# Kernel optimization log

Measured on AMD Instinct MI355X. Metric: run time of the kernel, lower is better.

Reference implementation:

```python
import jax, jax.numpy as jnp
import numpy as np

NU, NI, NR = 50000, 50000, 5   # users, items, rating levels
D, B, LS, LI = 64, 512, 32, 64 # embed_dim, batch, max social nbrs, max item hist
NEG = -1e9


def setup_inputs() -> dict:
    key = jax.random.key(0)
    ks = iter(jax.random.split(key, 64))
    def lin(din, dout):
        s = 1.0 / np.sqrt(din)
        return (jax.random.uniform(next(ks), (din, dout), minval=-s, maxval=s, dtype=jnp.float32),
                jax.random.uniform(next(ks), (dout,), minval=-s, maxval=s, dtype=jnp.float32))
    inp = {}
    inp['user_w'] = jax.random.normal(next(ks), (NU, D), dtype=jnp.float32) * 0.1
    inp['item_w'] = jax.random.normal(next(ks), (NI, D), dtype=jnp.float32) * 0.1
    inp['rating_w'] = jax.random.normal(next(ks), (NR, D), dtype=jnp.float32) * 0.1
    for name, din, dout in [('i_ln1', 2*D, D), ('i_ln2', D, D), ('i_ln3', 2*D, D),
                            ('i_att1', 2*D, D), ('i_att2', D, D), ('i_att3', D, 1),
                            ('s_ln1', D, D), ('s_ln2', 2*D, D), ('s_ln3', D, D),
                            ('s_att1', 2*D, D), ('s_att2', D, D), ('s_att3', D, 1)]:
        w, b = lin(din, dout)
        inp[name + '_w'] = w
        inp[name + '_b'] = b
    inp['nodes'] = jax.random.randint(next(ks), (B,), 0, NU)
    inp['social_hist'] = jax.random.randint(next(ks), (NU, LS), 0, NU)
    inp['social_mask'] = jax.random.bernoulli(next(ks), 0.5, (NU, LS)).at[:, 0].set(True)
    inp['item_hist'] = jax.random.randint(next(ks), (NU, LI), 0, NI)
    inp['rating_hist'] = jax.random.randint(next(ks), (NU, LI), 0, NR)
    inp['item_mask'] = jax.random.bernoulli(next(ks), 0.5, (NU, LI)).at[:, 0].set(True)
    return inp


def reference(user_w, item_w, rating_w,
              i_ln1_w, i_ln1_b, i_ln2_w, i_ln2_b, i_ln3_w, i_ln3_b,
              i_att1_w, i_att1_b, i_att2_w, i_att2_b, i_att3_w, i_att3_b,
              s_ln1_w, s_ln1_b, s_ln2_w, s_ln2_b, s_ln3_w, s_ln3_b,
              s_att1_w, s_att1_b, s_att2_w, s_att2_b, s_att3_w, s_att3_b,
              nodes, social_hist, social_mask, item_hist, rating_hist, item_mask):
    relu = jax.nn.relu

    def attn(x, w1, b1, w2, b2, w3, b3, mask):
        # x: [..., L, 2D] -> softmax weights over valid neighbors: [..., L]
        h = relu(x @ w1 + b1)
        h = relu(h @ w2 + b2)
        logit = (h @ w3 + b3)[..., 0]
        logit = jnp.where(mask, logit, NEG)
        return jax.nn.softmax(logit, axis=-1)

    def item_final(uids):
        # uids: any shape [...]; returns [..., D]  (Aggre_item.item_final)
        its, rts, m = item_hist[uids], rating_hist[uids], item_mask[uids]
        x = jnp.concatenate([item_w[its], rating_w[rts]], axis=-1)   # [...,LI,2D]
        x = relu(x @ i_ln1_w + i_ln1_b)                              # [...,LI,D]
        u = user_w[uids]                                             # [...,D]
        a_in = jnp.concatenate([x, jnp.broadcast_to(u[..., None, :], x.shape)], axis=-1)
        alpha = attn(a_in, i_att1_w, i_att1_b, i_att2_w, i_att2_b, i_att3_w, i_att3_b, m)
        hI = jnp.einsum('...l,...ld->...d', alpha, x)                # attention-weighted sum
        hI = relu(hI @ i_ln2_w + i_ln2_b)
        return relu(jnp.concatenate([u, hI], axis=-1) @ i_ln3_w + i_ln3_b)

    # item-space factor of query users
    hI_self = item_final(nodes)                                      # [B,D]
    # social aggregation: item_final over each user's social neighbors
    nbrs, nmask = social_hist[nodes], social_mask[nodes]             # [B,LS]
    hI_nb = item_final(nbrs)                                         # [B,LS,D]
    u = user_w[nodes]                                                # [B,D]
    b_in = jnp.concatenate([hI_nb, jnp.broadcast_to(u[:, None, :], hI_nb.shape)], axis=-1)
    beta = attn(b_in, s_att1_w, s_att1_b, s_att2_w, s_att2_b, s_att3_w, s_att3_b, nmask)
    hS = jnp.einsum('bl,bld->bd', beta, hI_nb)
    hS = relu(hS @ s_ln1_w + s_ln1_b)
    f = jnp.concatenate([hI_self, hS], axis=-1)
    f = relu(f @ s_ln2_w + s_ln2_b)
    return relu(f @ s_ln3_w + s_ln3_b)
```

## Files before the change

kernel.cpp:

```cpp
#include <hip/hip_runtime.h>
#include <math.h>


#define NII 50000
#define BB 512
#define LSS 32
#define NT 16896

typedef short short8 __attribute__((ext_vector_type(8)));
typedef float f32x4 __attribute__((ext_vector_type(4)));

static __device__ __forceinline__ bool mread(const void* p, long i, int mode) {
  if (mode == 0) return ((const int*)p)[i] != 0;
  if (mode == 2) return ((const float*)p)[i] != 0.0f;
  return ((const unsigned char*)p)[i] != 0;
}

static __device__ __forceinline__ float wsum(float v) {
#pragma unroll
  for (int s = 1; s < 64; s <<= 1) v += __shfl_xor(v, s);
  return v;
}
static __device__ __forceinline__ float wmax(float v) {
#pragma unroll
  for (int s = 1; s < 64; s <<= 1) v = fmaxf(v, __shfl_xor(v, s));
  return v;
}
static __device__ __forceinline__ float rsum16(float v) {
#pragma unroll
  for (int s = 1; s < 16; s <<= 1) v += __shfl_xor(v, s);
  return v;
}
static __device__ __forceinline__ float rmax16(float v) {
#pragma unroll
  for (int s = 1; s < 16; s <<= 1) v = fmaxf(v, __shfl_xor(v, s));
  return v;
}

static __device__ __forceinline__ short bf16rne(float f) {
  unsigned u = __float_as_uint(f);
  u = (u + 0x7FFFu + ((u >> 16) & 1u)) >> 16;
  return (short)u;
}
static __device__ __forceinline__ float bf16tof(short h) {
  return __uint_as_float(((unsigned)(unsigned short)h) << 16);
}

static __device__ __forceinline__ void wave_fence() {
  asm volatile("s_waitcnt lgkmcnt(0)" ::: "memory");
  __builtin_amdgcn_sched_barrier(0);
}

__global__ void setup_kernel(const unsigned int* __restrict__ sm,
                             int* __restrict__ flag,
                             const float* __restrict__ rating_w,
                             const float* __restrict__ w1,
                             const float* __restrict__ b1,
                             float* __restrict__ RW1g,
                             const float* __restrict__ A1w,
                             const float* __restrict__ A2w,
                             short* __restrict__ B1,
                             short* __restrict__ B2,
                             short* __restrict__ W1hi,
                             short* __restrict__ W1lo) {
  const int tid = threadIdx.x;
  if (blockIdx.x == 0) {
    __shared__ int notInt, notFloat;
    if (tid == 0) { notInt = 0; notFloat = 0; }
    __syncthreads();
    int ni = 0, nf = 0;
    for (int i = tid; i < 4096; i += 256) {
      unsigned int x = sm[i];
      if (x > 1u) ni = 1;
      if (x != 0u && x != 0x3F800000u) nf = 1;
    }
    if (ni) atomicOr(&notInt, 1);
    if (nf) atomicOr(&notFloat, 1);
    __syncthreads();
    if (tid == 0) flag[0] = notInt ? (notFloat ? 1 : 2) : 0;
  } else if (blockIdx.x == 1) {
    for (int t = tid; t < 320; t += 256) {
      const int r = t >> 6, c = t & 63;
      float acc = b1[c];
      for (int k = 0; k < 64; ++k)
        acc = fmaf(rating_w[r * 64 + k], w1[(64 + k) * 64 + c], acc);
      RW1g[r * 64 + c] = acc;
    }
  } else {
    for (int idx = tid; idx < 4096; idx += 256) {
      int e = idx & 7, g = idx >> 3;
      int l = g & 63, q = g >> 6;
      int kb = q >> 2, nb = q & 3;
      int k = kb * 32 + ((l >> 4) & 3) * 8 + e;
      int col = nb * 16 + (l & 15);
      B1[idx] = bf16rne(A1w[k * 64 + col]);
      B2[idx] = bf16rne(A2w[k * 64 + col]);
      float a = w1[k * 64 + col];
      short h = bf16rne(a);
      W1hi[idx] = h;
      W1lo[idx] = bf16rne(a - bf16tof(h));
    }
  }
}

__global__ void prepack2_kernel(const float* __restrict__ S1w,
                                const float* __restrict__ S2w,
                                short* __restrict__ B1,
                                short* __restrict__ B2) {
  for (int idx = threadIdx.x; idx < 4096; idx += 256) {
    int e = idx & 7, g = idx >> 3;
    int l = g & 63, q = g >> 6;
    int kb = q >> 2, nb = q & 3;
    int k = kb * 32 + ((l >> 4) & 3) * 8 + e;
    int col = nb * 16 + (l & 15);
    B1[idx] = bf16rne(S1w[k * 64 + col]);
    B2[idx] = bf16rne(S2w[k * 64 + col]);
  }
}

__global__ __launch_bounds__(256)
void pre_xbase_mfma_kernel(const float* __restrict__ item_w,
                           const short* __restrict__ W1hi,
                           const short* __restrict__ W1lo,
                           float* __restrict__ xbase) {
  const int lane = threadIdx.x & 63, w = threadIdx.x >> 6;
  const int l15 = lane & 15, lg4 = lane >> 4;
  short8 bh[8], bl[8];
#pragma unroll
  for (int q = 0; q < 8; ++q) {
    bh[q] = *(const short8*)(W1hi + (q * 64 + lane) * 8);
    bl[q] = *(const short8*)(W1lo + (q * 64 + lane) * 8);
  }
  const int wid = blockIdx.x * 4 + w;
  const int nw = gridDim.x * 4;
  for (int tile = wid; tile < 3125; tile += nw) {
    const long r0 = (long)tile * 16;
    const float* ap = item_w + (r0 + l15) * 64 + lg4 * 8;
    short8 ah[2], al[2];
#pragma unroll
    for (int kb = 0; kb < 2; ++kb) {
      const float4 a = *(const float4*)(ap + kb * 32);
      const float4 b = *(const float4*)(ap + kb * 32 + 4);
      float v[8] = {a.x, a.y, a.z, a.w, b.x, b.y, b.z, b.w};
      short8 hi, lo;
#pragma unroll
      for (int e = 0; e < 8; ++e) {
        short h = bf16rne(v[e]);
        hi[e] = h;
        lo[e] = bf16rne(v[e] - bf16tof(h));
      }
      ah[kb] = hi;
      al[kb] = lo;
    }
#pragma unroll
    for (int nb = 0; nb < 4; ++nb) {
      f32x4 acc = {0.0f, 0.0f, 0.0f, 0.0f};
      acc = __builtin_amdgcn_mfma_f32_16x16x32_bf16(ah[0], bh[0 * 4 + nb], acc, 0, 0, 0);
      acc = __builtin_amdgcn_mfma_f32_16x16x32_bf16(ah[1], bh[1 * 4 + nb], acc, 0, 0, 0);
      acc = __builtin_amdgcn_mfma_f32_16x16x32_bf16(ah[0], bl[0 * 4 + nb], acc, 0, 0, 0);
      acc = __builtin_amdgcn_mfma_f32_16x16x32_bf16(ah[1], bl[1 * 4 + nb], acc, 0, 0, 0);
      acc = __builtin_amdgcn_mfma_f32_16x16x32_bf16(al[0], bh[0 * 4 + nb], acc, 0, 0, 0);
      acc = __builtin_amdgcn_mfma_f32_16x16x32_bf16(al[1], bh[1 * 4 + nb], acc, 0, 0, 0);
#pragma unroll
      for (int r = 0; r < 4; ++r)
        xbase[(r0 + lg4 * 4 + r) * 64 + nb * 16 + l15] = acc[r];
    }
  }
}

__global__ void build_active_kernel(const int* __restrict__ nodes,
                                    const int* __restrict__ social_hist,
                                    const void* __restrict__ social_mask,
                                    const int* __restrict__ flagp,
                                    int* __restrict__ counter,
                                    int* __restrict__ list,
                                    int* __restrict__ aUid) {
  const int t = blockIdx.x * 256 + threadIdx.x;
  if (t >= NT) return;
  const int mode = flagp[0];
  int uid;
  bool active;
  if (t < BB) {
    active = true;
    uid = nodes[t];
  } else {
    int nb = t - BB;
    int b = nb >> 5, l = nb & 31;
    long mi = (long)nodes[b] * LSS + l;
    active = mread(social_mask, mi, mode);
    uid = active ? social_hist[mi] : 0;
  }
  if (active) {
    int pos = atomicAdd(counter, 1);
    list[pos] = t;
    aUid[pos] = uid;
  }
}

__global__ __launch_bounds__(256, 2)
void uA1_kernel(const float* __restrict__ user_w,
                const float* __restrict__ A1w, const float* __restrict__ A1b,
                const int* __restrict__ idxsrc, const int* __restrict__ nActp,
                float* __restrict__ uA1buf) {
  const int tid = threadIdx.x, lane = tid & 63, w = tid >> 6;
  const int i0 = blockIdx.x * 64;
  const int nA = nActp[0];
  if (i0 >= nA) return;
  __shared__ float sW[64][64], sU[64][64];
  __shared__ float sb[64];
  __shared__ int sUid[64];
  for (int i = tid; i < 4096; i += 256) sW[i >> 6][i & 63] = A1w[4096 + i];
  if (tid < 64) {
    sb[tid] = A1b[tid];
    sUid[tid] = (i0 + tid < nA) ? idxsrc[i0 + tid] : 0;
  }
  __syncthreads();
  for (int i = tid; i < 4096; i += 256) {
    int r = i >> 6, c = i & 63;
    sU[r][c] = user_w[(long)sUid[r] * 64 + c];
  }
  __syncthreads();
  float acc[16];
#pragma unroll
  for (int r = 0; r < 16; ++r) acc[r] = sb[lane];
  for (int k = 0; k < 64; k += 4) {
    float wv0 = sW[k][lane], wv1 = sW[k + 1][lane];
    float wv2 = sW[k + 2][lane], wv3 = sW[k + 3][lane];
#pragma unroll
    for (int r = 0; r < 16; ++r) {
      const float4 xv = *(const float4*)(&sU[w * 16 + r][k]);
      acc[r] = fmaf(xv.x, wv0, acc[r]);
      acc[r] = fmaf(xv.y, wv1, acc[r]);
      acc[r] = fmaf(xv.z, wv2, acc[r]);
      acc[r] = fmaf(xv.w, wv3, acc[r]);
    }
  }
#pragma unroll
  for (int r = 0; r < 16; ++r) {
    int row = i0 + w * 16 + r;
    if (row < nA) uA1buf[(long)row * 64 + lane] = acc[r];
  }
}

__global__ __launch_bounds__(512, 6)
void core_mfma_kernel(const float* __restrict__ xbase,
                      const float* __restrict__ RW1g,
                      const float* __restrict__ uA1buf,
                      const short* __restrict__ Bimg1,
                      const short* __restrict__ Bimg2,
                      const float* __restrict__ A2b,
                      const float* __restrict__ A3w,
                      const int* __restrict__ item_hist,
                      const int* __restrict__ rating_hist,
                      const void* __restrict__ item_mask,
                      const int* __restrict__ flagp,
                      const int* __restrict__ aUid,
                      const int* __restrict__ nActp,
                      float* __restrict__ hvecbuf) {
  __shared__ __align__(16) short sB1[4096], sB2[4096];
  __shared__ __align__(16) char smem[8][3072];
  const int tid = threadIdx.x, lane = tid & 63, w = tid >> 6;
  short* h1w = (short*)(smem[w]);
  float* lgw = (float*)(smem[w] + 2560);
  int* cw = (int*)(smem[w] + 2816);
  float* vAw = (float*)(smem[w]);

  ((int4*)sB1)[tid] = ((const int4*)Bimg1)[tid];
  ((int4*)sB2)[tid] = ((const int4*)Bimg2)[tid];
  __syncthreads();

  const int mode = flagp[0];
  const int nA = nActp[0];
  const float a2bv = A2b[lane];
  const float a3v = A3w[lane];
  const int l15 = lane & 15;
  const int lg4 = lane >> 4;

#define B1F(q) (*(const short8*)(sB1 + ((q) * 64 + lane) * 8))
#define B2F(q) (*(const short8*)(sB2 + ((q) * 64 + lane) * 8))

  for (int idx = blockIdx.x * 8 + w; idx < nA; idx += gridDim.x * 8) {
    wave_fence();
    const long uid = aUid[idx];

    const long mbase = uid * 64;
    bool mk = mread(item_mask, mbase + lane, mode);
    unsigned long long bal = __ballot(mk);
    const int nact = (int)__popcll(bal);
    int pos = (int)__popcll(bal & ((1ull << lane) - 1ull));
    if (mk) cw[pos] = (item_hist[mbase + lane] << 3) | rating_hist[mbase + lane];
    const float uA1v = uA1buf[(long)idx * 64 + lane];
    wave_fence();

    float m = -1e30f, s = 0.0f;
    float hIa[16];
#pragma unroll
    for (int q = 0; q < 16; ++q) hIa[q] = 0.0f;

    const int ng = (nact + 15) >> 4;
    for (int mc = 0; mc < ng; ++mc) {
      wave_fence();
      int row = mc * 16 + l15;
      const bool valid = (row < nact);
      if (row >= nact) row = nact - 1;
      const int p = cw[row];
      const long it = p >> 3;
      const int rt = p & 7;
      float xf[16];
#pragma unroll
      for (int kb = 0; kb < 2; ++kb) {
        const int koff = kb * 32 + lg4 * 8;
        const float* xp = xbase + it * 64 + koff;
        const float* rp = RW1g + rt * 64 + koff;
        const float4 a = *(const float4*)xp;
        const float4 b = *(const float4*)(xp + 4);
        const float4 c = *(const float4*)rp;
        const float4 d = *(const float4*)(rp + 4);
        xf[kb * 8 + 0] = fmaxf(a.x + c.x, 0.0f);
        xf[kb * 8 + 1] = fmaxf(a.y + c.y, 0.0f);
        xf[kb * 8 + 2] = fmaxf(a.z + c.z, 0.0f);
        xf[kb * 8 + 3] = fmaxf(a.w + c.w, 0.0f);
        xf[kb * 8 + 4] = fmaxf(b.x + d.x, 0.0f);
        xf[kb * 8 + 5] = fmaxf(b.y + d.y, 0.0f);
        xf[kb * 8 + 6] = fmaxf(b.z + d.z, 0.0f);
        xf[kb * 8 + 7] = fmaxf(b.w + d.w, 0.0f);
      }
      short8 xa[2];
#pragma unroll
      for (int kb = 0; kb < 2; ++kb) {
        short8 f;
#pragma unroll
        for (int e = 0; e < 8; ++e) f[e] = bf16rne(xf[kb * 8 + e]);
        xa[kb] = f;
      }
#pragma unroll
      for (int nb = 0; nb < 4; ++nb) {
        const float ui = __shfl(uA1v, nb * 16 + l15);
        f32x4 acc = {ui, ui, ui, ui};
        acc = __builtin_amdgcn_mfma_f32_16x16x32_bf16(xa[0], B1F(0 * 4 + nb), acc, 0, 0, 0);
        acc = __builtin_amdgcn_mfma_f32_16x16x32_bf16(xa[1], B1F(1 * 4 + nb), acc, 0, 0, 0);
#pragma unroll
        for (int r = 0; r < 4; ++r)
          h1w[(lg4 * 4 + r) * 80 + nb * 16 + l15] = bf16rne(fmaxf(acc[r], 0.0f));
      }
      wave_fence();
      short8 ha[2];
      ha[0] = *(const short8*)(h1w + l15 * 80 + lg4 * 8);
      ha[1] = *(const short8*)(h1w + l15 * 80 + 32 + lg4 * 8);
      float t0 = 0.0f, t1 = 0.0f, t2 = 0.0f, t3 = 0.0f;
#pragma unroll
      for (int nb = 0; nb < 4; ++nb) {
        const float b2 = __shfl(a2bv, nb * 16 + l15);
        f32x4 acc = {b2, b2, b2, b2};
        acc = __builtin_amdgcn_mfma_f32_16x16x32_bf16(ha[0], B2F(0 * 4 + nb), acc, 0, 0, 0);
        acc = __builtin_amdgcn_mfma_f32_16x16x32_bf16(ha[1], B2F(1 * 4 + nb), acc, 0, 0, 0);
        const float a3c = __shfl(a3v, nb * 16 + l15);
        t0 = fmaf(fmaxf(acc[0], 0.0f), a3c, t0);
        t1 = fmaf(fmaxf(acc[1], 0.0f), a3c, t1);
        t2 = fmaf(fmaxf(acc[2], 0.0f), a3c, t2);
        t3 = fmaf(fmaxf(acc[3], 0.0f), a3c, t3);
      }
      t0 = rsum16(t0); t1 = rsum16(t1); t2 = rsum16(t2); t3 = rsum16(t3);
      if (l15 == 0) {
        const int jb = lg4 * 4;
        lgw[jb + 0] = t0;
        lgw[jb + 1] = t1;
        lgw[jb + 2] = t2;
        lgw[jb + 3] = t3;
      }
      wave_fence();
      const float lv = valid ? lgw[l15] : -1e30f;
      const float cm = rmax16(lv);
      const float mn = fmaxf(m, cm);
      const float scale = __expf(m - mn);
      const float e = valid ? __expf(lv - mn) : 0.0f;
      const float cs = rsum16(e);
      s = s * scale + cs;
      m = mn;
#pragma unroll
      for (int q = 0; q < 16; ++q) hIa[q] = fmaf(hIa[q], scale, e * xf[q]);
    }
    wave_fence();

    const float inv = 1.0f / s;
#pragma unroll
    for (int q = 0; q < 16; ++q) hIa[q] = rsum16(hIa[q] * inv);
    if (l15 == 0) {
#pragma unroll
      for (int e = 0; e < 8; ++e) {
        vAw[lg4 * 8 + e] = hIa[e];
        vAw[32 + lg4 * 8 + e] = hIa[8 + e];
      }
    }
    wave_fence();
    hvecbuf[(long)idx * 64 + lane] = vAw[lane];
  }
#undef B1F
#undef B2F
}

__global__ __launch_bounds__(256, 2)
void hI2final_kernel(const float* __restrict__ hvecbuf,
                     const float* __restrict__ user_w,
                     const float* __restrict__ W2w, const float* __restrict__ W2b,
                     const float* __restrict__ W3w, const float* __restrict__ W3b,
                     const int* __restrict__ list, const int* __restrict__ aUid,
                     const int* __restrict__ nActp, float* __restrict__ hIbuf) {
  const int tid = threadIdx.x, lane = tid & 63, w = tid >> 6;
  const int i0 = blockIdx.x * 32;
  const int nA = nActp[0];
  if (i0 >= nA) return;
  __shared__ float sW[128][64];
  __shared__ float sX[32][128];
  __shared__ float sb[64];
  __shared__ int sUid[32], sInst[32];
  for (int i = tid; i < 4096; i += 256) sW[i >> 6][i & 63] = W2w[i];
  if (tid < 64) sb[tid] = W2b[tid];
  if (tid < 32) {
    bool ok = (i0 + tid) < nA;
    sUid[tid] = ok ? aUid[i0 + tid] : 0;
    sInst[tid] = ok ? list[i0 + tid] : 0;
  }
  __syncthreads();
  for (int i = tid; i < 2048; i += 256) {
    int r = i >> 6, c = i & 63;
    sX[r][64 + c] = (i0 + r < nA) ? hvecbuf[(long)(i0 + r) * 64 + c] : 0.0f;
    sX[r][c] = user_w[(long)sUid[r] * 64 + c];
  }
  __syncthreads();

  float acc[8];
  {
    const float bv = sb[lane];
#pragma unroll
    for (int r = 0; r < 8; ++r) acc[r] = bv;
    for (int k = 0; k < 64; k += 4) {
      float wv0 = sW[k][lane], wv1 = sW[k + 1][lane];
      float wv2 = sW[k + 2][lane], wv3 = sW[k + 3][lane];
#pragma unroll
      for (int r = 0; r < 8; ++r) {
        const float4 xv = *(const float4*)(&sX[w * 8 + r][64 + k]);
        acc[r] = fmaf(xv.x, wv0, acc[r]);
        acc[r] = fmaf(xv.y, wv1, acc[r]);
        acc[r] = fmaf(xv.z, wv2, acc[r]);
        acc[r] = fmaf(xv.w, wv3, acc[r]);
      }
    }
#pragma unroll
    for (int r = 0; r < 8; ++r) sX[w * 8 + r][64 + lane] = fmaxf(acc[r], 0.0f);
  }
  __syncthreads();
  for (int i = tid; i < 8192; i += 256) sW[i >> 6][i & 63] = W3w[i];
  if (tid < 64) sb[tid] = W3b[tid];
  __syncthreads();

  {
    const float bv = sb[lane];
#pragma unroll
    for (int r = 0; r < 8; ++r) acc[r] = bv;
    for (int k = 0; k < 128; k += 4) {
      float wv0 = sW[k][lane], wv1 = sW[k + 1][lane];
      float wv2 = sW[k + 2][lane], wv3 = sW[k + 3][lane];
#pragma unroll
      for (int r = 0; r < 8; ++r) {
        const float4 xv = *(const float4*)(&sX[w * 8 + r][k]);
        acc[r] = fmaf(xv.x, wv0, acc[r]);
        acc[r] = fmaf(xv.y, wv1, acc[r]);
        acc[r] = fmaf(xv.z, wv2, acc[r]);
        acc[r] = fmaf(xv.w, wv3, acc[r]);
      }
    }
#pragma unroll
    for (int r = 0; r < 8; ++r) {
      int row = i0 + w * 8 + r;
      if (row < nA)
        hIbuf[(long)sInst[w * 8 + r] * 64 + lane] = fmaxf(acc[r], 0.0f);
    }
  }
}

__global__ __launch_bounds__(256, 8)
void social_fused_kernel(const float* __restrict__ hIbuf,
                         const float* __restrict__ user_w,
                         const float* __restrict__ S1w,
                         const float* __restrict__ S1b,
                         const short* __restrict__ S1img,
                         const short* __restrict__ S2img,
                         const float* __restrict__ S2b,
                         const float* __restrict__ S3w,
                         const float* __restrict__ L1w, const float* __restrict__ L1b,
                         const float* __restrict__ L2w, const float* __restrict__ L2b,
                         const float* __restrict__ L3w, const float* __restrict__ L3b,
                         const int* __restrict__ nodes,
                         const void* __restrict__ social_mask,
                         const int* __restrict__ flagp,
                         float* __restrict__ out) {
  __shared__ __align__(16) short sB1[4096], sB2[4096];
  __shared__ __align__(16) char smem[4][3584];
  const int tid = threadIdx.x, lane = tid & 63, w = tid >> 6;
  short* h1w = (short*)(smem[w]);
  float* lgw = (float*)(smem[w] + 2560);
  int* cw = (int*)(smem[w] + 2816);
  float* vA = (float*)(smem[w] + 3072);
  float* vB = (float*)(smem[w] + 3328);

  for (int i = tid; i < 512; i += 256) {
    ((int4*)sB1)[i] = ((const int4*)S1img)[i];
    ((int4*)sB2)[i] = ((const int4*)S2img)[i];
  }
  __syncthreads();

  const int mode = flagp[0];
  const int l15 = lane & 15;
  const int lg4 = lane >> 4;
  const int b = blockIdx.x * 4 + w;
  const long uid = nodes[b];

  bool m = (lane < LSS) ? mread(social_mask, uid * LSS + lane, mode) : false;
  unsigned long long bal = __ballot(m);
  const int nval = (int)__popcll(bal);
  int pos = (int)__popcll(bal & ((1ull << lane) - 1ull));
  if (m) cw[pos] = lane;

  const float uv = user_w[uid * 64 + lane];
  float uA1v = S1b[lane];
#pragma unroll 8
  for (int k = 0; k < 64; ++k)
    uA1v = fmaf(__shfl(uv, k), S1w[(64 + k) * 64 + lane], uA1v);
  const float a2bv = S2b[lane];
  const float a3v = S3w[lane];
  wave_fence();

  const long hbase = 512L + (long)b * 32;
  const int ng = (nval + 15) >> 4;
  for (int mc = 0; mc < ng; ++mc) {
    wave_fence();
    int row = mc * 16 + l15;
    if (row >= nval) row = nval - 1;
    const long hrow = hbase + cw[row];
    short8 xa[2];
#pragma unroll
    for (int kb = 0; kb < 2; ++kb) {
      const float* xp = hIbuf + hrow * 64 + kb * 32 + lg4 * 8;
      const float4 a = *(const float4*)xp;
      const float4 bb = *(const float4*)(xp + 4);
      short8 f;
      f[0] = bf16rne(a.x);  f[1] = bf16rne(a.y);
      f[2] = bf16rne(a.z);  f[3] = bf16rne(a.w);
      f[4] = bf16rne(bb.x); f[5] = bf16rne(bb.y);
      f[6] = bf16rne(bb.z); f[7] = bf16rne(bb.w);
      xa[kb] = f;
    }
#pragma unroll
    for (int nb = 0; nb < 4; ++nb) {
      const float ui = __shfl(uA1v, nb * 16 + l15);
      f32x4 acc = {ui, ui, ui, ui};
      acc = __builtin_amdgcn_mfma_f32_16x16x32_bf16(
          xa[0], *(const short8*)(sB1 + ((0 * 4 + nb) * 64 + lane) * 8), acc, 0, 0, 0);
      acc = __builtin_amdgcn_mfma_f32_16x16x32_bf16(
          xa[1], *(const short8*)(sB1 + ((1 * 4 + nb) * 64 + lane) * 8), acc, 0, 0, 0);
#pragma unroll
      for (int r = 0; r < 4; ++r)
        h1w[(lg4 * 4 + r) * 80 + nb * 16 + l15] = bf16rne(fmaxf(acc[r], 0.0f));
    }
    wave_fence();
    short8 ha[2];
    ha[0] = *(const short8*)(h1w + l15 * 80 + lg4 * 8);
    ha[1] = *(const short8*)(h1w + l15 * 80 + 32 + lg4 * 8);
    float t0 = 0.0f, t1 = 0.0f, t2 = 0.0f, t3 = 0.0f;
#pragma unroll
    for (int nb = 0; nb < 4; ++nb) {
      const float b2 = __shfl(a2bv, nb * 16 + l15);
      f32x4 acc = {b2, b2, b2, b2};
      acc = __builtin_amdgcn_mfma_f32_16x16x32_bf16(
          ha[0], *(const short8*)(sB2 + ((0 * 4 + nb) * 64 + lane) * 8), acc, 0, 0, 0);
      acc = __builtin_amdgcn_mfma_f32_16x16x32_bf16(
          ha[1], *(const short8*)(sB2 + ((1 * 4 + nb) * 64 + lane) * 8), acc, 0, 0, 0);
      const float a3c = __shfl(a3v, nb * 16 + l15);
      t0 = fmaf(fmaxf(acc[0], 0.0f), a3c, t0);
      t1 = fmaf(fmaxf(acc[1], 0.0f), a3c, t1);
      t2 = fmaf(fmaxf(acc[2], 0.0f), a3c, t2);
      t3 = fmaf(fmaxf(acc[3], 0.0f), a3c, t3);
    }
    t0 = rsum16(t0); t1 = rsum16(t1); t2 = rsum16(t2); t3 = rsum16(t3);
    if (l15 == 0) {
      const int jb = mc * 16 + lg4 * 4;
      lgw[jb + 0] = t0;
      lgw[jb + 1] = t1;
      lgw[jb + 2] = t2;
      lgw[jb + 3] = t3;
    }
  }
  wave_fence();

  const bool valid = (lane < nval);
  float lv = valid ? lgw[lane] : -1e30f;
  float mx = wmax(lv);
  float e = valid ? __expf(lv - mx) : 0.0f;
  float s = wsum(e);
  const float beta = e / s;

  float hs = 0.0f;
  for (int j = 0; j < nval; ++j) {
    const float bj = __shfl(beta, j);
    hs = fmaf(bj, hIbuf[(hbase + cw[j]) * 64 + lane], hs);
  }

  vA[lane] = hs;
  wave_fence();
  float acc = L1b[lane];
#pragma unroll 8
  for (int k = 0; k < 64; ++k) acc = fmaf(vA[k], L1w[k * 64 + lane], acc);
  const float vecB = fmaxf(acc, 0.0f);
  const float selfv = hIbuf[(long)b * 64 + lane];
  wave_fence();
  vA[lane] = selfv;
  vB[lane] = vecB;
  wave_fence();
  acc = L2b[lane];
#pragma unroll 8
  for (int k = 0; k < 64; ++k) acc = fmaf(vA[k], L2w[k * 64 + lane], acc);
#pragma unroll 8
  for (int k = 0; k < 64; ++k) acc = fmaf(vB[k], L2w[(64 + k) * 64 + lane], acc);
  const float fv = fmaxf(acc, 0.0f);
  wave_fence();
  vA[lane] = fv;
  wave_fence();
  acc = L3b[lane];
#pragma unroll 8
  for (int k = 0; k < 64; ++k) acc = fmaf(vA[k], L3w[k * 64 + lane], acc);
  out[(long)b * 64 + lane] = fmaxf(acc, 0.0f);
}

extern "C" void kernel_launch(void* const* d_in, const int* in_sizes, int n_in,
                              void* d_out, int out_size, void* d_ws, size_t ws_size,
                              hipStream_t stream) {
  const float* user_w   = (const float*)d_in[0];
  const float* item_w   = (const float*)d_in[1];
  const float* rating_w = (const float*)d_in[2];
  const float* i_ln1_w  = (const float*)d_in[3];
  const float* i_ln1_b  = (const float*)d_in[4];
  const float* i_ln2_w  = (const float*)d_in[5];
  const float* i_ln2_b  = (const float*)d_in[6];
  const float* i_ln3_w  = (const float*)d_in[7];
  const float* i_ln3_b  = (const float*)d_in[8];
  const float* i_att1_w = (const float*)d_in[9];
  const float* i_att1_b = (const float*)d_in[10];
  const float* i_att2_w = (const float*)d_in[11];
  const float* i_att2_b = (const float*)d_in[12];
  const float* i_att3_w = (const float*)d_in[13];
  const float* i_att3_b = (const float*)d_in[14];
  const float* s_ln1_w  = (const float*)d_in[15];
  const float* s_ln1_b  = (const float*)d_in[16];
  const float* s_ln2_w  = (const float*)d_in[17];
  const float* s_ln2_b  = (const float*)d_in[18];
  const float* s_ln3_w  = (const float*)d_in[19];
  const float* s_ln3_b  = (const float*)d_in[20];
  const float* s_att1_w = (const float*)d_in[21];
  const float* s_att1_b = (const float*)d_in[22];
  const float* s_att2_w = (const float*)d_in[23];
  const float* s_att2_b = (const float*)d_in[24];
  const float* s_att3_w = (const float*)d_in[25];
  const float* s_att3_b = (const float*)d_in[26];
  const int*  nodes       = (const int*)d_in[27];
  const int*  social_hist = (const int*)d_in[28];
  const void* social_mask = d_in[29];
  const int*  item_hist   = (const int*)d_in[30];
  const int*  rating_hist = (const int*)d_in[31];
  const void* item_mask   = d_in[32];

  char* ws = (char*)d_ws;
  int*   flag    = (int*)(ws + 0);
  int*   counter = (int*)(ws + 256);
  int*   list    = (int*)(ws + 512);
  int*   aUid    = (int*)(ws + 68096);
  float* uA1buf  = (float*)(ws + 135680);
  float* hvecbuf = (float*)(ws + 4461056);
  float* hIbuf   = hvecbuf;
  short* W1hi    = (short*)(ws + 4461056);
  short* W1lo    = (short*)(ws + 4469248);
  float* xbase   = (float*)(ws + 8786432);
  short* S1img   = (short*)(ws + 8786432);
  short* S2img   = (short*)(ws + 8794624);
  float* RW1g    = (float*)(ws + 21586432);
  short* Bimg1   = (short*)(ws + 21587712);
  short* Bimg2   = (short*)(ws + 21595904);

  hipMemsetAsync(counter, 0, 4, stream);
  setup_kernel<<<3, 256, 0, stream>>>((const unsigned int*)social_mask, flag,
                                      rating_w, i_ln1_w, i_ln1_b, RW1g,
                                      i_att1_w, i_att2_w, Bimg1, Bimg2, W1hi, W1lo);
  pre_xbase_mfma_kernel<<<512, 256, 0, stream>>>(item_w, W1hi, W1lo, xbase);
  build_active_kernel<<<NT / 256, 256, 0, stream>>>(
      nodes, social_hist, social_mask, flag, counter, list, aUid);
  uA1_kernel<<<NT / 64, 256, 0, stream>>>(user_w, i_att1_w, i_att1_b,
                                          aUid, counter, uA1buf);
  core_mfma_kernel<<<NT / 16, 512, 0, stream>>>(
      xbase, RW1g, uA1buf, Bimg1, Bimg2, i_att2_b, i_att3_w,
      item_hist, rating_hist, item_mask, flag, aUid, counter, hvecbuf);
  prepack2_kernel<<<1, 256, 0, stream>>>(s_att1_w, s_att2_w, S1img, S2img);
  hI2final_kernel<<<NT / 32, 256, 0, stream>>>(
      hvecbuf, user_w, i_ln2_w, i_ln2_b, i_ln3_w, i_ln3_b,
      list, aUid, counter, hIbuf);
  social_fused_kernel<<<BB / 4, 256, 0, stream>>>(
      hIbuf, user_w, s_att1_w, s_att1_b, S1img, S2img, s_att2_b, s_att3_w,
      s_ln1_w, s_ln1_b, s_ln2_w, s_ln2_b, s_ln3_w, s_ln3_b,
      nodes, social_mask, flag, (float*)d_out);
}
```

Measured before the change: 127.9 us.

## Software-pipeline item gathers across chunks in core MFMA attention kernel

Replaces the per-chunk loop with a fully unrolled four-chunk schedule that issues the global loads of the gathered item rows one or two chunks ahead of their MFMA processing, so memory latency overlaps with compute. Attention logits are now redistributed with lane shuffles instead of an LDS round trip. The weighted sum now uses the bf16-rounded inputs rather than the fp32 values. Blocks shrink from 512 to 256 threads with a different occupancy hint. The unroll assumes at most 64 active history entries per user (LI=64), and the extra live registers may lower occupancy.

New measurement: 129.5 us. About the same (+1.2%).

```diff
diff --git a/kernel.cpp b/kernel.cpp
--- a/kernel.cpp
+++ b/kernel.cpp
@@ -242,7 +242,7 @@
   }
 }
 
-__global__ __launch_bounds__(512, 6)
+__global__ __launch_bounds__(256, 5)
 void core_mfma_kernel(const float* __restrict__ xbase,
                       const float* __restrict__ RW1g,
                       const float* __restrict__ uA1buf,
@@ -258,15 +258,16 @@
                       const int* __restrict__ nActp,
                       float* __restrict__ hvecbuf) {
   __shared__ __align__(16) short sB1[4096], sB2[4096];
-  __shared__ __align__(16) char smem[8][3072];
+  __shared__ __align__(16) char smem[4][3072];
   const int tid = threadIdx.x, lane = tid & 63, w = tid >> 6;
   short* h1w = (short*)(smem[w]);
-  float* lgw = (float*)(smem[w] + 2560);
-  int* cw = (int*)(smem[w] + 2816);
+  int* cw = (int*)(smem[w] + 2560);
   float* vAw = (float*)(smem[w]);
 
-  ((int4*)sB1)[tid] = ((const int4*)Bimg1)[tid];
-  ((int4*)sB2)[tid] = ((const int4*)Bimg2)[tid];
+  for (int i = tid; i < 512; i += 256) {
+    ((int4*)sB1)[i] = ((const int4*)Bimg1)[i];
+    ((int4*)sB2)[i] = ((const int4*)Bimg2)[i];
+  }
   __syncthreads();
 
   const int mode = flagp[0];
@@ -279,7 +280,90 @@
 #define B1F(q) (*(const short8*)(sB1 + ((q) * 64 + lane) * 8))
 #define B2F(q) (*(const short8*)(sB2 + ((q) * 64 + lane) * 8))
 
-  for (int idx = blockIdx.x * 8 + w; idx < nA; idx += gridDim.x * 8) {
+#define ISSUEX(C, A0, B0, A1, B1)                                           \
+  if ((C) < ng) {                                                           \
+    const float* xp = xbase + (long)(pk##C >> 3) * 64 + lg4 * 8;            \
+    A0 = *(const float4*)(xp);                                              \
+    B0 = *(const float4*)(xp + 4);                                          \
+    A1 = *(const float4*)(xp + 32);                                         \
+    B1 = *(const float4*)(xp + 36);                                         \
+  }
+
+#define CONVX(C, A0, B0, A1, B1, XL, XH)                                    \
+  if ((C) < ng) {                                                           \
+    const float* rp = RW1g + (pk##C & 7) * 64 + lg4 * 8;                    \
+    const float4 c0 = *(const float4*)(rp);                                 \
+    const float4 d0 = *(const float4*)(rp + 4);                             \
+    const float4 c1 = *(const float4*)(rp + 32);                            \
+    const float4 d1 = *(const float4*)(rp + 36);                            \
+    XL[0] = bf16rne(fmaxf(A0.x + c0.x, 0.0f));                              \
+    XL[1] = bf16rne(fmaxf(A0.y + c0.y, 0.0f));                              \
+    XL[2] = bf16rne(fmaxf(A0.z + c0.z, 0.0f));                              \
+    XL[3] = bf16rne(fmaxf(A0.w + c0.w, 0.0f));                              \
+    XL[4] = bf16rne(fmaxf(B0.x + d0.x, 0.0f));                              \
+    XL[5] = bf16rne(fmaxf(B0.y + d0.y, 0.0f));                              \
+    XL[6] = bf16rne(fmaxf(B0.z + d0.z, 0.0f));                              \
+    XL[7] = bf16rne(fmaxf(B0.w + d0.w, 0.0f));                              \
+    XH[0] = bf16rne(fmaxf(A1.x + c1.x, 0.0f));                              \
+    XH[1] = bf16rne(fmaxf(A1.y + c1.y, 0.0f));                              \
+    XH[2] = bf16rne(fmaxf(A1.z + c1.z, 0.0f));                              \
+    XH[3] = bf16rne(fmaxf(A1.w + c1.w, 0.0f));                              \
+    XH[4] = bf16rne(fmaxf(B1.x + d1.x, 0.0f));                              \
+    XH[5] = bf16rne(fmaxf(B1.y + d1.y, 0.0f));                              \
+    XH[6] = bf16rne(fmaxf(B1.z + d1.z, 0.0f));                              \
+    XH[7] = bf16rne(fmaxf(B1.w + d1.w, 0.0f));                              \
+  }
+
+#define PROCC(C, XL, XH)                                                    \
+  if ((C) < ng) {                                                           \
+    const bool vld = ((C)*16 + l15) < nact;                                 \
+    wave_fence();                      \
+    _Pragma("unroll")                                                       \
+    for (int nb = 0; nb < 4; ++nb) {                                        \
+      const float ui = __shfl(uA1v, nb * 16 + l15);                         \
+      f32x4 acc = {ui, ui, ui, ui};                                         \
+      acc = __builtin_amdgcn_mfma_f32_16x16x32_bf16(XL, B1F(nb), acc, 0, 0, 0); \
+      acc = __builtin_amdgcn_mfma_f32_16x16x32_bf16(XH, B1F(4 + nb), acc, 0, 0, 0); \
+      _Pragma("unroll")                                                     \
+      for (int r = 0; r < 4; ++r)                                           \
+        h1w[(lg4 * 4 + r) * 80 + nb * 16 + l15] = bf16rne(fmaxf(acc[r], 0.0f)); \
+    }                                                                       \
+    wave_fence();                                                           \
+    const short8 ha0 = *(const short8*)(h1w + l15 * 80 + lg4 * 8);          \
+    const short8 ha1 = *(const short8*)(h1w + l15 * 80 + 32 + lg4 * 8);     \
+    float t0 = 0.0f, t1 = 0.0f, t2 = 0.0f, t3 = 0.0f;                       \
+    _Pragma("unroll")                                                       \
+    for (int nb = 0; nb < 4; ++nb) {                                        \
+      const float b2 = __shfl(a2bv, nb * 16 + l15);                         \
+      f32x4 acc = {b2, b2, b2, b2};                                         \
+      acc = __builtin_amdgcn_mfma_f32_16x16x32_bf16(ha0, B2F(nb), acc, 0, 0, 0); \
+      acc = __builtin_amdgcn_mfma_f32_16x16x32_bf16(ha1, B2F(4 + nb), acc, 0, 0, 0); \
+      const float a3c = __shfl(a3v, nb * 16 + l15);                         \
+      t0 = fmaf(fmaxf(acc[0], 0.0f), a3c, t0);                              \
+      t1 = fmaf(fmaxf(acc[1], 0.0f), a3c, t1);                              \
+      t2 = fmaf(fmaxf(acc[2], 0.0f), a3c, t2);                              \
+      t3 = fmaf(fmaxf(acc[3], 0.0f), a3c, t3);                              \
+    }                                                                       \
+    t0 = rsum16(t0); t1 = rsum16(t1); t2 = rsum16(t2); t3 = rsum16(t3);     \
+    const int srcl = ((l15 >> 2) << 4) | l15;                               \
+    const float v0 = __shfl(t0, srcl), v1 = __shfl(t1, srcl);               \
+    const float v2 = __shfl(t2, srcl), v3 = __shfl(t3, srcl);               \
+    float lv = (l15 & 2) ? ((l15 & 1) ? v3 : v2) : ((l15 & 1) ? v1 : v0);   \
+    lv = vld ? lv : -1e30f;                                                 \
+    const float cm = rmax16(lv);                                            \
+    const float mn = fmaxf(m, cm);                                          \
+    const float scale = __expf(m - mn);                                     \
+    const float e = vld ? __expf(lv - mn) : 0.0f;                           \
+    s = s * scale + rsum16(e);                                              \
+    m = mn;                                                                 \
+    _Pragma("unroll")                                                       \
+    for (int q = 0; q < 8; ++q) {                                           \
+      hIa[q] = fmaf(hIa[q], scale, e * bf16tof(XL[q]));                     \
+      hIa[8 + q] = fmaf(hIa[8 + q], scale, e * bf16tof(XH[q]));             \
+    }                                                                       \
+  }
+
+  for (int idx = blockIdx.x * 4 + w; idx < nA; idx += gridDim.x * 4) {
     wave_fence();
     const long uid = aUid[idx];
 
@@ -292,94 +376,32 @@
     const float uA1v = uA1buf[(long)idx * 64 + lane];
     wave_fence();
 
+    const int ng = (nact + 15) >> 4;
+    const int pk0 = cw[min(0 * 16 + l15, nact - 1)];
+    const int pk1 = cw[min(1 * 16 + l15, nact - 1)];
+    const int pk2 = cw[min(2 * 16 + l15, nact - 1)];
+    const int pk3 = cw[min(3 * 16 + l15, nact - 1)];
+
     float m = -1e30f, s = 0.0f;
     float hIa[16];
 #pragma unroll
     for (int q = 0; q < 16; ++q) hIa[q] = 0.0f;
 
-    const int ng = (nact + 15) >> 4;
-    for (int mc = 0; mc < ng; ++mc) {
-      wave_fence();
-      int row = mc * 16 + l15;
-      const bool valid = (row < nact);
-      if (row >= nact) row = nact - 1;
-      const int p = cw[row];
-      const long it = p >> 3;
-      const int rt = p & 7;
-      float xf[16];
-#pragma unroll
-      for (int kb = 0; kb < 2; ++kb) {
-        const int koff = kb * 32 + lg4 * 8;
-        const float* xp = xbase + it * 64 + koff;
-        const float* rp = RW1g + rt * 64 + koff;
-        const float4 a = *(const float4*)xp;
-        const float4 b = *(const float4*)(xp + 4);
-        const float4 c = *(const float4*)rp;
-        const float4 d = *(const float4*)(rp + 4);
-        xf[kb * 8 + 0] = fmaxf(a.x + c.x, 0.0f);
-        xf[kb * 8 + 1] = fmaxf(a.y + c.y, 0.0f);
-        xf[kb * 8 + 2] = fmaxf(a.z + c.z, 0.0f);
-        xf[kb * 8 + 3] = fmaxf(a.w + c.w, 0.0f);
-        xf[kb * 8 + 4] = fmaxf(b.x + d.x, 0.0f);
-        xf[kb * 8 + 5] = fmaxf(b.y + d.y, 0.0f);
-        xf[kb * 8 + 6] = fmaxf(b.z + d.z, 0.0f);
-        xf[kb * 8 + 7] = fmaxf(b.w + d.w, 0.0f);
-      }
-      short8 xa[2];
-#pragma unroll
-      for (int kb = 0; kb < 2; ++kb) {
-        short8 f;
-#pragma unroll
-        for (int e = 0; e < 8; ++e) f[e] = bf16rne(xf[kb * 8 + e]);
-        xa[kb] = f;
-      }
-#pragma unroll
-      for (int nb = 0; nb < 4; ++nb) {
-        const float ui = __shfl(uA1v, nb * 16 + l15);
-        f32x4 acc = {ui, ui, ui, ui};
-        acc = __builtin_amdgcn_mfma_f32_16x16x32_bf16(xa[0], B1F(0 * 4 + nb), acc, 0, 0, 0);
-        acc = __builtin_amdgcn_mfma_f32_16x16x32_bf16(xa[1], B1F(1 * 4 + nb), acc, 0, 0, 0);
-#pragma unroll
-        for (int r = 0; r < 4; ++r)
-          h1w[(lg4 * 4 + r) * 80 + nb * 16 + l15] = bf16rne(fmaxf(acc[r], 0.0f));
-      }
-      wave_fence();
-      short8 ha[2];
-      ha[0] = *(const short8*)(h1w + l15 * 80 + lg4 * 8);
-      ha[1] = *(const short8*)(h1w + l15 * 80 + 32 + lg4 * 8);
-      float t0 = 0.0f, t1 = 0.0f, t2 = 0.0f, t3 = 0.0f;
-#pragma unroll
-      for (int nb = 0; nb < 4; ++nb) {
-        const float b2 = __shfl(a2bv, nb * 16 + l15);
-        f32x4 acc = {b2, b2, b2, b2};
-        acc = __builtin_amdgcn_mfma_f32_16x16x32_bf16(ha[0], B2F(0 * 4 + nb), acc, 0, 0, 0);
-        acc = __builtin_amdgcn_mfma_f32_16x16x32_bf16(ha[1], B2F(1 * 4 + nb), acc, 0, 0, 0);
-        const float a3c = __shfl(a3v, nb * 16 + l15);
-        t0 = fmaf(fmaxf(acc[0], 0.0f), a3c, t0);
-        t1 = fmaf(fmaxf(acc[1], 0.0f), a3c, t1);
-        t2 = fmaf(fmaxf(acc[2], 0.0f), a3c, t2);
-        t3 = fmaf(fmaxf(acc[3], 0.0f), a3c, t3);
-      }
-      t0 = rsum16(t0); t1 = rsum16(t1); t2 = rsum16(t2); t3 = rsum16(t3);
-      if (l15 == 0) {
-        const int jb = lg4 * 4;
-        lgw[jb + 0] = t0;
-        lgw[jb + 1] = t1;
-        lgw[jb + 2] = t2;
-        lgw[jb + 3] = t3;
-      }
-      wave_fence();
-      const float lv = valid ? lgw[l15] : -1e30f;
-      const float cm = rmax16(lv);
-      const float mn = fmaxf(m, cm);
-      const float scale = __expf(m - mn);
-      const float e = valid ? __expf(lv - mn) : 0.0f;
-      const float cs = rsum16(e);
-      s = s * scale + cs;
-      m = mn;
-#pragma unroll
-      for (int q = 0; q < 16; ++q) hIa[q] = fmaf(hIa[q], scale, e * xf[q]);
-    }
+    float4 ra0, rb0, ra1, rb1;
+    float4 sa0, sb0, sa1, sb1;
+    short8 xl, xh;
+    ISSUEX(0, ra0, rb0, ra1, rb1);
+    ISSUEX(1, sa0, sb0, sa1, sb1);
+    CONVX(0, ra0, rb0, ra1, rb1, xl, xh);
+    ISSUEX(2, ra0, rb0, ra1, rb1);
+    PROCC(0, xl, xh);
+    CONVX(1, sa0, sb0, sa1, sb1, xl, xh);
+    ISSUEX(3, sa0, sb0, sa1, sb1);
+    PROCC(1, xl, xh);
+    CONVX(2, ra0, rb0, ra1, rb1, xl, xh);
+    PROCC(2, xl, xh);
+    CONVX(3, sa0, sb0, sa1, sb1, xl, xh);
+    PROCC(3, xl, xh);
     wave_fence();
 
     const float inv = 1.0f / s;
@@ -397,6 +419,9 @@
   }
 #undef B1F
 #undef B2F
+#undef ISSUEX
+#undef CONVX
+#undef PROCC
 }
 
 __global__ __launch_bounds__(256, 2)
@@ -695,7 +720,7 @@
       nodes, social_hist, social_mask, flag, counter, list, aUid);
   uA1_kernel<<<NT / 64, 256, 0, stream>>>(user_w, i_att1_w, i_att1_b,
                                           aUid, counter, uA1buf);
-  core_mfma_kernel<<<NT / 16, 512, 0, stream>>>(
+  core_mfma_kernel<<<NT / 8, 256, 0, stream>>>(
       xbase, RW1g, uA1buf, Bimg1, Bimg2, i_att2_b, i_att3_w,
       item_hist, rating_hist, item_mask, flag, aUid, counter, hvecbuf);
   prepack2_kernel<<<1, 256, 0, stream>>>(s_att1_w, s_att2_w, S1img, S2img);
```
